# Optimization experiments

Hardware: AMD Instinct MI355X
Metric: run time of the kernel (lower is better)

Reference implementation:

```python
import jax, jax.numpy as jnp
import numpy as np

N, F, C = 4096, 512, 512
NUM_HOPS, TOP_K, MASK_RATIO = 3, 8, 0.5
EPS = 1e-12


def setup_inputs() -> dict:
    key = jax.random.key(0)
    ks = jax.random.split(key, 8)
    return {
        "x": jax.random.normal(ks[0], (N, F), dtype=jnp.float32),
        "adj": jax.random.uniform(ks[1], (NUM_HOPS, N, N), dtype=jnp.float32),
        "rand_mask": jax.random.uniform(ks[2], (NUM_HOPS, N, N), dtype=jnp.float32),
        "W_in": jax.random.normal(ks[3], (F, C), dtype=jnp.float32) * 0.02,
        "b_in": jnp.zeros((C,), dtype=jnp.float32),
        "W_out": jax.random.normal(ks[4], (C, C), dtype=jnp.float32) * 0.02,
        "b_out": jnp.zeros((C,), dtype=jnp.float32),
        "alpha": jnp.ones((NUM_HOPS,), dtype=jnp.float32),
        "beta": jnp.full((1,), 0.5, dtype=jnp.float32),
    }


def reference(x, adj, rand_mask, W_in, b_in, W_out, b_out, alpha, beta):
    H_low = x @ W_in + b_in  # (N, C)
    # F.normalize(x, dim=-1) @ F.normalize(x.T, dim=0) == x_n @ x_n.T
    xn = x / jnp.maximum(jnp.linalg.norm(x, axis=-1, keepdims=True), EPS)
    sim = xn @ xn.T  # (N, N)
    a = jax.nn.softmax(alpha)
    rows = jnp.arange(N)[:, None]
    H_high = jnp.zeros((N, F), dtype=x.dtype)
    for k in range(NUM_HOPS):
        Akw = a[k] * adj[k] * sim  # (N, N)
        _, idx = jax.lax.top_k(Akw, TOP_K)  # (N, TOP_K)
        topk_mask = jnp.zeros_like(Akw).at[rows, idx].set(1.0)
        retain = (rand_mask[k] < MASK_RATIO).astype(Akw.dtype)
        final_mask = ((topk_mask + retain) > 0).astype(Akw.dtype)
        Hk = (Akw * final_mask) @ x  # (N, F)
        H_high = H_high + a[k] * Hk
    b = beta[0]
    H = jax.nn.relu(b * H_low + (1.0 - b) * H_high)
    # dropout in eval mode (identity)
    out = H @ W_out + b_out
    return jax.nn.log_softmax(out, axis=-1)
```

## Files before the change

### kernel.cpp

```cpp
#include <hip/hip_runtime.h>
#include <hip/hip_bf16.h>
#include <stdint.h>

#define NROW 4096
#define FDIM 512

typedef short bf16x8 __attribute__((ext_vector_type(8)));
typedef float f32x4 __attribute__((ext_vector_type(4)));
typedef float f4 __attribute__((ext_vector_type(4)));
typedef ushort u16x4 __attribute__((ext_vector_type(4)));

#define NEG_INF (-__builtin_inff())

__device__ inline ushort f2bf(float f) {
    union { float f; uint32_t u; } c{f};
    uint32_t u = c.u;
    uint32_t r = (u + 0x7FFF + ((u >> 16) & 1)) >> 16;
    return (ushort)r;
}
__device__ inline float bf2f(ushort h) {
    union { uint32_t u; float f; } c{((uint32_t)h) << 16};
    return c.f;
}
__device__ inline uint32_t cvt_pk_bf16(float lo, float hi) {
    uint32_t r;
    asm("v_cvt_pk_bf16_f32 %0, %1, %2" : "=v"(r) : "v"(lo), "v"(hi));
    return r;
}
__device__ inline float up0(uint32_t p) {
    union { uint32_t u; float f; } c{p << 16}; return c.f;
}
__device__ inline float up1(uint32_t p) {
    union { uint32_t u; float f; } c{p & 0xFFFF0000u}; return c.f;
}

__device__ inline float waveReduceMax(float v) {
    #pragma unroll
    for (int o = 32; o > 0; o >>= 1) v = fmaxf(v, __shfl_xor(v, o));
    return v;
}
__device__ inline float waveReduceSum(float v) {
    #pragma unroll
    for (int o = 32; o > 0; o >>= 1) v += __shfl_xor(v, o);
    return v;
}

__device__ inline void CE(float& a, float& b) {
    float mx = fmaxf(a, b);
    b = fminf(a, b);
    a = mx;
}
__device__ inline void sort8(float (&l)[8]) {
    CE(l[0],l[1]); CE(l[2],l[3]); CE(l[4],l[5]); CE(l[6],l[7]);
    CE(l[0],l[2]); CE(l[1],l[3]); CE(l[4],l[6]); CE(l[5],l[7]);
    CE(l[1],l[2]); CE(l[5],l[6]);
    CE(l[0],l[4]); CE(l[1],l[5]); CE(l[2],l[6]); CE(l[3],l[7]);
    CE(l[2],l[4]); CE(l[3],l[5]);
    CE(l[1],l[2]); CE(l[3],l[4]); CE(l[5],l[6]);
}
__device__ inline void mergeTop8(float (&a)[8], const float (&b)[8]) {
    float t[8];
    #pragma unroll
    for (int i = 0; i < 8; i++) t[i] = fmaxf(a[i], b[7 - i]);
    CE(t[0],t[4]); CE(t[1],t[5]); CE(t[2],t[6]); CE(t[3],t[7]);
    CE(t[0],t[2]); CE(t[1],t[3]); CE(t[4],t[6]); CE(t[5],t[7]);
    CE(t[0],t[1]); CE(t[2],t[3]); CE(t[4],t[5]); CE(t[6],t[7]);
    #pragma unroll
    for (int i = 0; i < 8; i++) a[i] = t[i];
}

#define GLL16(src, dst)                                                        \
    __builtin_amdgcn_global_load_lds(                                          \
        (const __attribute__((address_space(1))) void*)(src),                  \
        (__attribute__((address_space(3))) void*)(dst), 16, 0, 0)

__global__ __launch_bounds__(64) void coef_k(const float* __restrict__ alpha,
                                             const float* __restrict__ beta,
                                             float* __restrict__ coef) {
    if (threadIdx.x == 0) {
        float a0 = alpha[0], a1 = alpha[1], a2 = alpha[2];
        float m = fmaxf(a0, fmaxf(a1, a2));
        float e0 = expf(a0 - m), e1 = expf(a1 - m), e2 = expf(a2 - m);
        float s = e0 + e1 + e2;
        coef[0] = e0 / s; coef[1] = e1 / s; coef[2] = e2 / s;
        coef[3] = beta[0];
    }
}

__global__ __launch_bounds__(256) void prep_x(const float* __restrict__ x,
                                              ushort* __restrict__ xn,
                                              ushort* __restrict__ xb) {
    int row = blockIdx.x, tid = threadIdx.x;
    int lane = tid & 63, w = tid >> 6;
    const float* xr = x + (size_t)row * FDIM;
    float v0 = xr[tid], v1 = xr[tid + 256];
    float ss = v0 * v0 + v1 * v1;
    ss = waveReduceSum(ss);
    __shared__ float b4[4];
    if (lane == 0) b4[w] = ss;
    __syncthreads();
    float tot = b4[0] + b4[1] + b4[2] + b4[3];
    float inv = 1.f / fmaxf(sqrtf(tot), 1e-12f);
    size_t o = (size_t)row * FDIM + tid;
    xn[o] = f2bf(v0 * inv);  xn[o + 256] = f2bf(v1 * inv);
    xb[o] = f2bf(v0);        xb[o + 256] = f2bf(v1);
}

__global__ __launch_bounds__(256) void transpose_xb(const ushort* __restrict__ in,
                                                    ushort* __restrict__ out) {
    __shared__ ushort t[64][65];
    int lx = threadIdx.x & 63, ly = threadIdx.x >> 6;
    int c0 = blockIdx.x * 64, r0 = blockIdx.y * 64;
    #pragma unroll
    for (int i = 0; i < 16; i++)
        t[ly + 4 * i][lx] = in[(size_t)(r0 + ly + 4 * i) * FDIM + c0 + lx];
    __syncthreads();
    #pragma unroll
    for (int i = 0; i < 16; i++)
        out[(size_t)(c0 + ly + 4 * i) * NROW + r0 + lx] = t[lx][ly + 4 * i];
}

__global__ __launch_bounds__(256) void convT_w(const float* __restrict__ Wf,
                                               ushort* __restrict__ WT) {
    __shared__ ushort t[64][65];
    int lx = threadIdx.x & 63, ly = threadIdx.x >> 6;
    int c0 = blockIdx.x * 64, r0 = blockIdx.y * 64;
    #pragma unroll
    for (int i = 0; i < 16; i++)
        t[ly + 4 * i][lx] = f2bf(Wf[(size_t)(r0 + ly + 4 * i) * 512 + c0 + lx]);
    __syncthreads();
    #pragma unroll
    for (int i = 0; i < 16; i++)
        WT[(size_t)(c0 + ly + 4 * i) * 512 + r0 + lx] = t[lx][ly + 4 * i];
}

template <int EPI>
__global__ __launch_bounds__(256) void gemm_abT(
    const ushort* __restrict__ A, int lda,
    const ushort* __restrict__ B, int ldb,
    int Kdim, int ldc,
    float* __restrict__ Cf, ushort* __restrict__ Cb,
    const float* __restrict__ bias) {
    constexpr int BK = 64;
    constexpr int NT = 128 * BK;
    constexpr int CPR = BK / 8;
    constexpr int PASSES = (128 * CPR) / 256;
    __shared__ __align__(16) ushort smem[2 * NT];
    ushort* As = smem;
    ushort* Bs = smem + NT;

    if constexpr (EPI == 3) {
        A += (size_t)blockIdx.z * 1024;
        B += (size_t)blockIdx.z * 1024;
        Cf += (size_t)blockIdx.z * ((size_t)NROW * 512);
    }

    const int tid = threadIdx.x;
    const int lane = tid & 63, w = tid >> 6;
    const int wr = w >> 1, wc = w & 1;
    const int m0 = blockIdx.y * 128;
    const int n0 = blockIdx.x * 128;

    f32x4 acc[4][4];
    #pragma unroll
    for (int mi = 0; mi < 4; mi++)
        #pragma unroll
        for (int ni = 0; ni < 4; ni++)
            #pragma unroll
            for (int r = 0; r < 4; r++) acc[mi][ni][r] = 0.f;

    for (int k0 = 0; k0 < Kdim; k0 += BK) {
        #pragma unroll
        for (int p = 0; p < PASSES; ++p) {
            int chunk = p * 256 + tid;
            int row = chunk / CPR;
            int kc = chunk % CPR;
            const ushort* asrc = A + (size_t)(m0 + row) * lda + k0 + kc * 8;
            const ushort* bsrc = B + (size_t)(n0 + row) * ldb + k0 + kc * 8;
            ushort* abase = As + (size_t)(p * 256 + w * 64) * 8;
            ushort* bbase = Bs + (size_t)(p * 256 + w * 64) * 8;
            GLL16(asrc, abase);
            GLL16(bsrc, bbase);
        }
        __syncthreads();
        #pragma unroll
        for (int kf = 0; kf < BK / 32; ++kf) {
            const int ko = kf * 32 + (lane >> 4) * 8;
            bf16x8 av[4], bv[4];
            #pragma unroll
            for (int mi = 0; mi < 4; mi++)
                av[mi] = *(const bf16x8*)&As[(wr * 64 + mi * 16 + (lane & 15)) * BK + ko];
            #pragma unroll
            for (int ni = 0; ni < 4; ni++)
                bv[ni] = *(const bf16x8*)&Bs[(wc * 64 + ni * 16 + (lane & 15)) * BK + ko];
            #pragma unroll
            for (int mi = 0; mi < 4; mi++)
                #pragma unroll
                for (int ni = 0; ni < 4; ni++)
                    acc[mi][ni] = __builtin_amdgcn_mfma_f32_16x16x32_bf16(
                        av[mi], bv[ni], acc[mi][ni], 0, 0, 0);
        }
        __syncthreads();
    }

    #pragma unroll
    for (int mi = 0; mi < 4; mi++) {
        #pragma unroll
        for (int ni = 0; ni < 4; ni++) {
            int col = n0 + wc * 64 + ni * 16 + (lane & 15);
            #pragma unroll
            for (int r = 0; r < 4; r++) {
                int rowg = m0 + wr * 64 + mi * 16 + (lane >> 4) * 4 + r;
                size_t off = (size_t)rowg * ldc + col;
                float v = acc[mi][ni][r];
                if constexpr (EPI == 1) {
                    Cf[off] = v + bias[col];
                } else if constexpr (EPI == 3) {
                    Cf[off] = v;
                } else {
                    Cb[off] = f2bf(v);
                }
            }
        }
    }
}

__global__ __launch_bounds__(256) void topk_build_M(
    const ushort* __restrict__ simb, const float* __restrict__ adj,
    const float* __restrict__ rmask, const float* __restrict__ coef,
    ushort* __restrict__ Mout) {
    const int tid = threadIdx.x;
    const int lane = tid & 63;
    const int w = tid >> 6;
    const int rloc = w >> 1;
    const int half = w & 1;
    const int row = blockIdx.x * 2 + rloc;
    const int qbase = half * 8;
    __shared__ float wl[3][2][2][8];

    const int laneoff = lane * 4;

    const ushort* srow = simb + (size_t)row * NROW;
    uint2 svp[8];
    #pragma unroll
    for (int q = 0; q < 8; q++)
        svp[q] = *(const uint2*)(srow + (qbase + q) * 256 + laneoff);

    float macc[8][4];
    #pragma unroll
    for (int q = 0; q < 8; q++)
        #pragma unroll
        for (int c = 0; c < 4; c++) macc[q][c] = 0.f;

    for (int k = 0; k < 3; ++k) {
        const float* arow = adj + ((size_t)k * NROW + row) * NROW;
        const float* rrow = rmask + ((size_t)k * NROW + row) * NROW;

        uint2 avp[8];
        uint32_t rbits = 0;
        float l[8];

        #pragma unroll
        for (int ch = 0; ch < 4; ch++) {
            float v[8];
            #pragma unroll
            for (int qq = 0; qq < 2; qq++) {
                const int q = ch * 2 + qq;
                f4 a = *(const f4*)(arow + (qbase + q) * 256 + laneoff);
                f4 r = *(const f4*)(rrow + (qbase + q) * 256 + laneoff);
                uint32_t p0 = cvt_pk_bf16(a.x, a.y);
                uint32_t p1 = cvt_pk_bf16(a.z, a.w);
                avp[q].x = p0; avp[q].y = p1;
                rbits |= (r.x < 0.5f ? 1u : 0u) << (q * 4 + 0);
                rbits |= (r.y < 0.5f ? 1u : 0u) << (q * 4 + 1);
                rbits |= (r.z < 0.5f ? 1u : 0u) << (q * 4 + 2);
                rbits |= (r.w < 0.5f ? 1u : 0u) << (q * 4 + 3);
                v[qq * 4 + 0] = up0(p0) * up0(svp[q].x);
                v[qq * 4 + 1] = up1(p0) * up1(svp[q].x);
                v[qq * 4 + 2] = up0(p1) * up0(svp[q].y);
                v[qq * 4 + 3] = up1(p1) * up1(svp[q].y);
            }
            sort8(v);
            if (ch == 0) {
                #pragma unroll
                for (int i = 0; i < 8; i++) l[i] = v[i];
            } else {
                mergeTop8(l, v);
            }
        }

        #pragma unroll
        for (int lvl = 0; lvl < 6; lvl++) {
            float b[8];
            #pragma unroll
            for (int i = 0; i < 8; i++) b[i] = __shfl_xor(l[i], 1 << lvl);
            mergeTop8(l, b);
        }

        if (lane < 8) wl[k][rloc][half][lane] = l[lane];
        __syncthreads();
        {
            float b[8];
            #pragma unroll
            for (int i = 0; i < 8; i++) b[i] = wl[k][rloc][half ^ 1][i];
            mergeTop8(l, b);
        }
        const float thr = l[7];

        const float ak = coef[k];
        const float aksq = ak * ak;
        #pragma unroll
        for (int q = 0; q < 8; q++) {
            float av0 = up0(avp[q].x), av1 = up1(avp[q].x);
            float av2 = up0(avp[q].y), av3 = up1(avp[q].y);
            float s0 = up0(svp[q].x), s1 = up1(svp[q].x);
            float s2 = up0(svp[q].y), s3 = up1(svp[q].y);
            bool m0 = ((rbits >> (q * 4 + 0)) & 1) || (av0 * s0 >= thr);
            bool m1 = ((rbits >> (q * 4 + 1)) & 1) || (av1 * s1 >= thr);
            bool m2 = ((rbits >> (q * 4 + 2)) & 1) || (av2 * s2 >= thr);
            bool m3 = ((rbits >> (q * 4 + 3)) & 1) || (av3 * s3 >= thr);
            macc[q][0] += m0 ? aksq * av0 : 0.f;
            macc[q][1] += m1 ? aksq * av1 : 0.f;
            macc[q][2] += m2 ? aksq * av2 : 0.f;
            macc[q][3] += m3 ? aksq * av3 : 0.f;
        }
    }

    ushort* mrow = Mout + (size_t)row * NROW;
    #pragma unroll
    for (int q = 0; q < 8; q++) {
        u16x4 o;
        o[0] = f2bf(up0(svp[q].x) * macc[q][0]);
        o[1] = f2bf(up1(svp[q].x) * macc[q][1]);
        o[2] = f2bf(up0(svp[q].y) * macc[q][2]);
        o[3] = f2bf(up1(svp[q].y) * macc[q][3]);
        *(u16x4*)(mrow + (qbase + q) * 256 + laneoff) = o;
    }
}

__global__ __launch_bounds__(256) void reduce_relu(
    const float* __restrict__ parts, const float* __restrict__ hlow,
    const float* __restrict__ coef, ushort* __restrict__ Hb) {
    const size_t i = (size_t)blockIdx.x * 256 + threadIdx.x;
    const f4* p4 = (const f4*)parts;
    f4 s = p4[i];
    #pragma unroll
    for (int z = 1; z < 4; z++) s += p4[(size_t)z * 524288 + i];
    f4 hl = ((const f4*)hlow)[i];
    float cb = coef[3];
    u16x4 o;
    #pragma unroll
    for (int c = 0; c < 4; c++) {
        float h = cb * hl[c] + (1.f - cb) * s[c];
        o[c] = f2bf(fmaxf(h, 0.f));
    }
    *((u16x4*)Hb + i) = o;
}

__global__ __launch_bounds__(256) void logsoftmax_k(const float* __restrict__ L,
                                                    float* __restrict__ out) {
    int row = blockIdx.x, tid = threadIdx.x;
    int lane = tid & 63, w = tid >> 6;
    const float* lr = L + (size_t)row * 512;
    float v0 = lr[tid], v1 = lr[tid + 256];
    __shared__ float bm[4], bs[4];
    float m = fmaxf(v0, v1);
    m = waveReduceMax(m);
    if (lane == 0) bm[w] = m;
    __syncthreads();
    float M = fmaxf(fmaxf(bm[0], bm[1]), fmaxf(bm[2], bm[3]));
    float s = expf(v0 - M) + expf(v1 - M);
    s = waveReduceSum(s);
    if (lane == 0) bs[w] = s;
    __syncthreads();
    float S = bs[0] + bs[1] + bs[2] + bs[3];
    float lse = M + logf(S);
    float* orow = out + (size_t)row * 512;
    orow[tid] = v0 - lse;
    orow[tid + 256] = v1 - lse;
}

extern "C" void kernel_launch(void* const* d_in, const int* in_sizes, int n_in,
                              void* d_out, int out_size, void* d_ws, size_t ws_size,
                              hipStream_t stream) {
    const float* x     = (const float*)d_in[0];
    const float* adj   = (const float*)d_in[1];
    const float* rmask = (const float*)d_in[2];
    const float* W_in  = (const float*)d_in[3];
    const float* b_in  = (const float*)d_in[4];
    const float* W_out = (const float*)d_in[5];
    const float* b_out = (const float*)d_in[6];
    const float* alpha = (const float*)d_in[7];
    const float* beta  = (const float*)d_in[8];
    float* out = (float*)d_out;

    const size_t MB = 1024 * 1024;
    char* wsb = (char*)d_ws;
    ushort* simb   = (ushort*)wsb;
    float*  parts  = (float*)wsb;
    float*  logits = (float*)wsb;
    ushort* Mb     = (ushort*)(wsb + 32 * MB);
    ushort* xn     = (ushort*)(wsb + 64 * MB);
    ushort* xb     = (ushort*)(wsb + 68 * MB);
    ushort* xbT    = (ushort*)(wsb + 72 * MB);
    ushort* WinT   = (ushort*)(wsb + 76 * MB);
    ushort* WoutT  = (ushort*)(wsb + 76 * MB + 512 * 1024);
    float*  Hlow   = (float*)(wsb + 77 * MB);
    ushort* Hb     = (ushort*)(wsb + 85 * MB);
    float*  coef   = (float*)(wsb + 89 * MB);

    coef_k<<<1, 64, 0, stream>>>(alpha, beta, coef);
    prep_x<<<NROW, 256, 0, stream>>>(x, xn, xb);
    transpose_xb<<<dim3(8, 64), 256, 0, stream>>>(xb, xbT);
    convT_w<<<dim3(8, 8), 256, 0, stream>>>(W_in, WinT);
    convT_w<<<dim3(8, 8), 256, 0, stream>>>(W_out, WoutT);

    gemm_abT<4><<<dim3(32, 32), 256, 0, stream>>>(
        xn, FDIM, xn, FDIM, FDIM, NROW, nullptr, simb, nullptr);

    topk_build_M<<<NROW / 2, 256, 0, stream>>>(simb, adj, rmask, coef, Mb);

    gemm_abT<1><<<dim3(4, 32), 256, 0, stream>>>(
        xb, FDIM, WinT, FDIM, FDIM, 512, Hlow, nullptr, b_in);

    gemm_abT<3><<<dim3(4, 32, 4), 256, 0, stream>>>(
        Mb, NROW, xbT, NROW, 1024, 512, parts, nullptr, nullptr);

    reduce_relu<<<2048, 256, 0, stream>>>(parts, Hlow, coef, Hb);

    gemm_abT<1><<<dim3(4, 32), 256, 0, stream>>>(
        Hb, 512, WoutT, 512, 512, 512, logits, nullptr, b_out);

    logsoftmax_k<<<NROW, 256, 0, stream>>>(logits, out);
}
```

Before: 217.1 us.

## Split each top-k row across four waves with one row per block

The top-k mask kernel now assigns one row per block, with four waves each handling a 1024-column slice, instead of two waves per row and two rows per block. This halves the per-thread register footprint and doubles the block count, and issues all adj/rand_mask loads up front to improve latency hiding. Launch bounds now request higher occupancy. The trade-off is a four-way cross-wave merge through shared memory per hop, plus more blocks to schedule.

```diff
diff --git a/kernel.cpp b/kernel.cpp
--- a/kernel.cpp
+++ b/kernel.cpp
@@ -225,92 +225,101 @@
     }
 }
 
-__global__ __launch_bounds__(256) void topk_build_M(
+__global__ __launch_bounds__(256, 6) void topk_build_M(
     const ushort* __restrict__ simb, const float* __restrict__ adj,
     const float* __restrict__ rmask, const float* __restrict__ coef,
     ushort* __restrict__ Mout) {
     const int tid = threadIdx.x;
     const int lane = tid & 63;
     const int w = tid >> 6;
-    const int rloc = w >> 1;
-    const int half = w & 1;
-    const int row = blockIdx.x * 2 + rloc;
-    const int qbase = half * 8;
-    __shared__ float wl[3][2][2][8];
-
-    const int laneoff = lane * 4;
-
-    const ushort* srow = simb + (size_t)row * NROW;
-    uint2 svp[8];
-    #pragma unroll
-    for (int q = 0; q < 8; q++)
-        svp[q] = *(const uint2*)(srow + (qbase + q) * 256 + laneoff);
-
-    float macc[8][4];
-    #pragma unroll
-    for (int q = 0; q < 8; q++)
+    const int row = blockIdx.x;
+    __shared__ float wl[3][4][8];
+
+    const int cbase = w * 1024 + lane * 4;
+
+    const ushort* srow = simb + (size_t)row * NROW + cbase;
+    uint2 svp[4];
+    #pragma unroll
+    for (int q = 0; q < 4; q++)
+        svp[q] = *(const uint2*)(srow + q * 256);
+
+    float macc[4][4];
+    #pragma unroll
+    for (int q = 0; q < 4; q++)
         #pragma unroll
         for (int c = 0; c < 4; c++) macc[q][c] = 0.f;
 
     for (int k = 0; k < 3; ++k) {
-        const float* arow = adj + ((size_t)k * NROW + row) * NROW;
-        const float* rrow = rmask + ((size_t)k * NROW + row) * NROW;
-
-        uint2 avp[8];
+        const float* arow = adj + ((size_t)k * NROW + row) * NROW + cbase;
+        const float* rrow = rmask + ((size_t)k * NROW + row) * NROW + cbase;
+
+        f4 rv[4], a[4];
+        #pragma unroll
+        for (int q = 0; q < 4; q++) rv[q] = *(const f4*)(rrow + q * 256);
+        #pragma unroll
+        for (int q = 0; q < 4; q++) a[q] = *(const f4*)(arow + q * 256);
+
         uint32_t rbits = 0;
-        float l[8];
-
-        #pragma unroll
-        for (int ch = 0; ch < 4; ch++) {
-            float v[8];
-            #pragma unroll
-            for (int qq = 0; qq < 2; qq++) {
-                const int q = ch * 2 + qq;
-                f4 a = *(const f4*)(arow + (qbase + q) * 256 + laneoff);
-                f4 r = *(const f4*)(rrow + (qbase + q) * 256 + laneoff);
-                uint32_t p0 = cvt_pk_bf16(a.x, a.y);
-                uint32_t p1 = cvt_pk_bf16(a.z, a.w);
-                avp[q].x = p0; avp[q].y = p1;
-                rbits |= (r.x < 0.5f ? 1u : 0u) << (q * 4 + 0);
-                rbits |= (r.y < 0.5f ? 1u : 0u) << (q * 4 + 1);
-                rbits |= (r.z < 0.5f ? 1u : 0u) << (q * 4 + 2);
-                rbits |= (r.w < 0.5f ? 1u : 0u) << (q * 4 + 3);
-                v[qq * 4 + 0] = up0(p0) * up0(svp[q].x);
-                v[qq * 4 + 1] = up1(p0) * up1(svp[q].x);
-                v[qq * 4 + 2] = up0(p1) * up0(svp[q].y);
-                v[qq * 4 + 3] = up1(p1) * up1(svp[q].y);
-            }
-            sort8(v);
-            if (ch == 0) {
-                #pragma unroll
-                for (int i = 0; i < 8; i++) l[i] = v[i];
-            } else {
-                mergeTop8(l, v);
-            }
-        }
+        #pragma unroll
+        for (int q = 0; q < 4; q++) {
+            rbits |= (rv[q].x < 0.5f ? 1u : 0u) << (q * 4 + 0);
+            rbits |= (rv[q].y < 0.5f ? 1u : 0u) << (q * 4 + 1);
+            rbits |= (rv[q].z < 0.5f ? 1u : 0u) << (q * 4 + 2);
+            rbits |= (rv[q].w < 0.5f ? 1u : 0u) << (q * 4 + 3);
+        }
+
+        uint2 avp[4];
+        #pragma unroll
+        for (int q = 0; q < 4; q++) {
+            avp[q].x = cvt_pk_bf16(a[q].x, a[q].y);
+            avp[q].y = cvt_pk_bf16(a[q].z, a[q].w);
+        }
+
+        float lo8[8], hi8[8];
+        #pragma unroll
+        for (int qq = 0; qq < 2; qq++) {
+            lo8[qq * 4 + 0] = up0(avp[qq].x) * up0(svp[qq].x);
+            lo8[qq * 4 + 1] = up1(avp[qq].x) * up1(svp[qq].x);
+            lo8[qq * 4 + 2] = up0(avp[qq].y) * up0(svp[qq].y);
+            lo8[qq * 4 + 3] = up1(avp[qq].y) * up1(svp[qq].y);
+        }
+        #pragma unroll
+        for (int qq = 0; qq < 2; qq++) {
+            const int q = 2 + qq;
+            hi8[qq * 4 + 0] = up0(avp[q].x) * up0(svp[q].x);
+            hi8[qq * 4 + 1] = up1(avp[q].x) * up1(svp[q].x);
+            hi8[qq * 4 + 2] = up0(avp[q].y) * up0(svp[q].y);
+            hi8[qq * 4 + 3] = up1(avp[q].y) * up1(svp[q].y);
+        }
+        sort8(lo8);
+        sort8(hi8);
+        mergeTop8(lo8, hi8);
 
         #pragma unroll
         for (int lvl = 0; lvl < 6; lvl++) {
             float b[8];
             #pragma unroll
-            for (int i = 0; i < 8; i++) b[i] = __shfl_xor(l[i], 1 << lvl);
-            mergeTop8(l, b);
-        }
-
-        if (lane < 8) wl[k][rloc][half][lane] = l[lane];
+            for (int i = 0; i < 8; i++) b[i] = __shfl_xor(lo8[i], 1 << lvl);
+            mergeTop8(lo8, b);
+        }
+
+        if (lane < 8) wl[k][w][lane] = lo8[lane];
         __syncthreads();
-        {
-            float b[8];
-            #pragma unroll
-            for (int i = 0; i < 8; i++) b[i] = wl[k][rloc][half ^ 1][i];
-            mergeTop8(l, b);
-        }
-        const float thr = l[7];
+        #pragma unroll
+        for (int ww = 0; ww < 4; ww++) {
+            if (ww != w) {
+                float b[8];
+                #pragma unroll
+                for (int i = 0; i < 8; i++) b[i] = wl[k][ww][i];
+                mergeTop8(lo8, b);
+            }
+        }
+        const float thr = lo8[7];
 
         const float ak = coef[k];
         const float aksq = ak * ak;
         #pragma unroll
-        for (int q = 0; q < 8; q++) {
+        for (int q = 0; q < 4; q++) {
             float av0 = up0(avp[q].x), av1 = up1(avp[q].x);
             float av2 = up0(avp[q].y), av3 = up1(avp[q].y);
             float s0 = up0(svp[q].x), s1 = up1(svp[q].x);
@@ -326,15 +335,15 @@
         }
     }
 
-    ushort* mrow = Mout + (size_t)row * NROW;
-    #pragma unroll
-    for (int q = 0; q < 8; q++) {
+    ushort* mrow = Mout + (size_t)row * NROW + cbase;
+    #pragma unroll
+    for (int q = 0; q < 4; q++) {
         u16x4 o;
         o[0] = f2bf(up0(svp[q].x) * macc[q][0]);
         o[1] = f2bf(up1(svp[q].x) * macc[q][1]);
         o[2] = f2bf(up0(svp[q].y) * macc[q][2]);
         o[3] = f2bf(up1(svp[q].y) * macc[q][3]);
-        *(u16x4*)(mrow + (qbase + q) * 256 + laneoff) = o;
+        *(u16x4*)(mrow + q * 256) = o;
     }
 }
 
@@ -418,7 +427,7 @@
     gemm_abT<4><<<dim3(32, 32), 256, 0, stream>>>(
         xn, FDIM, xn, FDIM, FDIM, NROW, nullptr, simb, nullptr);
 
-    topk_build_M<<<NROW / 2, 256, 0, stream>>>(simb, adj, rmask, coef, Mb);
+    topk_build_M<<<NROW, 256, 0, stream>>>(simb, adj, rmask, coef, Mb);
 
     gemm_abT<1><<<dim3(4, 32), 256, 0, stream>>>(
         xb, FDIM, WinT, FDIM, FDIM, 512, Hlow, nullptr, b_in);
```

Result: slower. 278.6 us (+28.3%).
